# Performance work log

Hardware: AMD Instinct MI355X
Metric: run time of the kernel (lower is better)

The kernel has to match this reference:

```python
import jax, jax.numpy as jnp
import numpy as np
import math

EMBED = 1024
FF = 4096
HEADS = 16
HEAD = EMBED // HEADS
EPS = 1e-5


def new_gelu(x):
    c = math.sqrt(2.0 / math.pi)
    return 0.5 * x * (1.0 + jnp.tanh(c * (x + 0.044715 * x ** 3)))


def layer_norm(x, g, b):
    mu = jnp.mean(x, axis=-1, keepdims=True)
    var = jnp.var(x, axis=-1, keepdims=True)
    return (x - mu) * jax.lax.rsqrt(var + EPS) * g + b


def setup_inputs() -> dict:
    key = jax.random.key(0)
    ks = jax.random.split(key, 16)
    s = 0.02
    d = {
        'x': jax.random.normal(ks[0], (2, 2048, EMBED), jnp.float32),
        'Wq': jax.random.normal(ks[1], (EMBED, EMBED)) * s,
        'bq': jnp.zeros((EMBED,)),
        'Wk': jax.random.normal(ks[2], (EMBED, EMBED)) * s,
        'bk': jnp.zeros((EMBED,)),
        'Wv': jax.random.normal(ks[3], (EMBED, EMBED)) * s,
        'bv': jnp.zeros((EMBED,)),
        'Wp': jax.random.normal(ks[4], (EMBED, EMBED)) * s,
        'bp': jnp.zeros((EMBED,)),
        'W1': jax.random.normal(ks[5], (EMBED, FF)) * s,
        'b1': jnp.zeros((FF,)),
        'W2': jax.random.normal(ks[6], (FF, EMBED)) * s,
        'b2': jnp.zeros((EMBED,)),
        'g1': jnp.ones((EMBED,)), 'be1': jnp.zeros((EMBED,)),
        'g2': jnp.ones((EMBED,)), 'be2': jnp.zeros((EMBED,)),
    }
    return d


def reference(x, Wq, bq, Wk, bk, Wv, bv, Wp, bp, W1, b1, W2, b2, g1, be1, g2, be2):
    B, S, D = x.shape
    h = layer_norm(x, g1, be1)
    # project and split heads: [B,S,D] -> [B,H,S,Hd]
    def heads(y):
        return y.reshape(B, S, HEADS, HEAD).transpose(0, 2, 1, 3)
    Q = heads(h @ Wq + bq)
    K = heads(h @ Wk + bk)
    V = heads(h @ Wv + bv)
    att = jnp.einsum('bhqd,bhkd->bhqk', Q, K) / math.sqrt(HEAD)
    att = jax.nn.softmax(att, axis=-1)
    out = jnp.einsum('bhqk,bhkd->bhqd', att, V)
    out = out.transpose(0, 2, 1, 3).reshape(B, S, D)
    x = x + (out @ Wp + bp)  # dropout p=0 / eval -> identity
    h2 = layer_norm(x, g2, be2)
    x = x + (new_gelu(h2 @ W1 + b1) @ W2 + b2)
    return x
```

## Files before the change

### kernel.cpp

```cpp
#include <hip/hip_runtime.h>
#include <cstdint>


typedef __attribute__((ext_vector_type(8))) short short8;
typedef __attribute__((ext_vector_type(4))) float f32x4;

#define QSCL 0.18033688011112042f

__device__ __forceinline__ float bf2f(unsigned short u) {
    union { unsigned int i; float f; } v; v.i = ((unsigned int)u) << 16; return v.f;
}
__device__ __forceinline__ unsigned short f2bf(float f) {
    union { float f; unsigned int i; } v; v.f = f;
    unsigned int u = v.i;
    u += 0x7fff + ((u >> 16) & 1);
    return (unsigned short)(u >> 16);
}
__device__ __forceinline__ float gelu_f(float x) {
    float u = 0.7978845608028654f * (x + 0.044715f * x * x * x);
    float t = 1.f - 2.f / (__expf(2.f * u) + 1.f);
    return 0.5f * x * (1.f + t);
}
__device__ __forceinline__ void async16(const unsigned short* gp, unsigned short* lp) {
    __builtin_amdgcn_global_load_lds(
        (__attribute__((address_space(1))) void*)(gp),
        (__attribute__((address_space(3))) void*)(lp),
        16, 0, 0);
}

__device__ __forceinline__ void ln_dev(
    const float* __restrict__ x, const float* __restrict__ g,
    const float* __restrict__ b, unsigned short* __restrict__ o,
    int row, float* red)
{
    const int tid = threadIdx.x;
    const float4 v = ((const float4*)(x + (size_t)row * 1024))[tid];
    float f0 = v.x, f1 = v.y, f2 = v.z, f3 = v.w;
    float sum = f0 + f1 + f2 + f3;
    float sq  = f0 * f0 + f1 * f1 + f2 * f2 + f3 * f3;
    for (int off = 1; off < 64; off <<= 1) {
        sum += __shfl_xor(sum, off);
        sq  += __shfl_xor(sq,  off);
    }
    int wv = tid >> 6, ln = tid & 63;
    if (ln == 0) { red[wv] = sum; red[4 + wv] = sq; }
    __syncthreads();
    sum = red[0] + red[1] + red[2] + red[3];
    sq  = red[4] + red[5] + red[6] + red[7];
    float mu  = sum * (1.0f / 1024.0f);
    float var = sq  * (1.0f / 1024.0f) - mu * mu;
    float rsd = rsqrtf(fmaxf(var, 0.f) + 1e-5f);
    const float4 gg = ((const float4*)g)[tid];
    const float4 bb = ((const float4*)b)[tid];
    unsigned short* orow = o + (size_t)row * 1024;
    orow[4 * tid + 0] = f2bf((f0 - mu) * rsd * gg.x + bb.x);
    orow[4 * tid + 1] = f2bf((f1 - mu) * rsd * gg.y + bb.y);
    orow[4 * tid + 2] = f2bf((f2 - mu) * rsd * gg.z + bb.z);
    orow[4 * tid + 3] = f2bf((f3 - mu) * rsd * gg.w + bb.w);
}

__device__ __forceinline__ void transpose_dev(
    const float* __restrict__ in, unsigned short* __restrict__ out,
    int R, int C, int inStride, int bx, int by, unsigned short* tile ,
    float scale)
{
    const int tx = threadIdx.x & 15, ty = threadIdx.x >> 4;
    const int c0 = bx * 64, r0 = by * 64;
#pragma unroll
    for (int i = 0; i < 4; ++i) {
        int r = ty + 16 * i;
        float4 v = *(const float4*)(in + (size_t)(r0 + r) * inStride + c0 + tx * 4);
        tile[r * 70 + tx * 4 + 0] = f2bf(v.x * scale);
        tile[r * 70 + tx * 4 + 1] = f2bf(v.y * scale);
        tile[r * 70 + tx * 4 + 2] = f2bf(v.z * scale);
        tile[r * 70 + tx * 4 + 3] = f2bf(v.w * scale);
    }
    __syncthreads();
#pragma unroll
    for (int i = 0; i < 4; ++i) {
        int c = ty * 4 + i;
        ushort4 o;
        o.x = tile[(tx * 4 + 0) * 70 + c];
        o.y = tile[(tx * 4 + 1) * 70 + c];
        o.z = tile[(tx * 4 + 2) * 70 + c];
        o.w = tile[(tx * 4 + 3) * 70 + c];
        *(ushort4*)(out + (size_t)(c0 + c) * R + r0 + tx * 4) = o;
    }
}

__global__ __launch_bounds__(256) void ln_k(
    const float* __restrict__ x, const float* __restrict__ g,
    const float* __restrict__ b, unsigned short* __restrict__ o)
{
    __shared__ float red[8];
    ln_dev(x, g, b, o, blockIdx.x, red);
}
__global__ __launch_bounds__(256) void transpose_f2b(
    const float* __restrict__ in, unsigned short* __restrict__ out,
    int R, int C, int inStride, float scale)
{
    __shared__ unsigned short tile[64 * 70];
    transpose_dev(in, out, R, C, inStride, blockIdx.x, blockIdx.y, tile, scale);
}

__global__ __launch_bounds__(256) void prep1_k(
    const float* __restrict__ x,
    const float* __restrict__ g1, const float* __restrict__ be1,
    const float* __restrict__ Wq, const float* __restrict__ Wk,
    const float* __restrict__ Wv,
    const float* __restrict__ bq, const float* __restrict__ bk,
    const float* __restrict__ bv,
    unsigned short* __restrict__ hb,
    unsigned short* __restrict__ WTqkv,
    float* __restrict__ bcat)
{
    __shared__ unsigned short smem[64 * 70];
    const int b = blockIdx.x;
    if (b < 4096) {
        ln_dev(x, g1, be1, hb, b, (float*)smem);
    } else if (b < 4096 + 768) {
        int t = b - 4096;
        int w = t >> 8;
        int tt = t & 255;
        const float* W = (w == 0) ? Wq : (w == 1) ? Wk : Wv;
        transpose_dev(W, WTqkv + (size_t)w * 1024 * 1024,
                      1024, 1024, 1024, tt & 15, tt >> 4, smem,
                      (w == 0) ? QSCL : 1.f);
    } else {
        int i = (b - 4096 - 768) * 256 + threadIdx.x;
        float v = (i < 1024) ? bq[i] * QSCL : (i < 2048) ? bk[i - 1024] : bv[i - 2048];
        bcat[i] = v;
    }
}

__global__ __launch_bounds__(256) void prep2_k(
    const float* __restrict__ x1,
    const float* __restrict__ g2, const float* __restrict__ be2,
    const float* __restrict__ W1, const float* __restrict__ W2,
    unsigned short* __restrict__ h2,
    unsigned short* __restrict__ WT1,
    unsigned short* __restrict__ WT2)
{
    __shared__ unsigned short smem[64 * 70];
    const int b = blockIdx.x;
    if (b < 4096) {
        ln_dev(x1, g2, be2, h2, b, (float*)smem);
    } else if (b < 4096 + 1024) {
        int t = b - 4096;
        transpose_dev(W1, WT1, 1024, 4096, 4096, t & 63, t >> 6, smem, 1.f);
    } else {
        int t = b - 4096 - 1024;
        transpose_dev(W2, WT2, 4096, 1024, 1024, t & 15, t >> 4, smem, 1.f);
    }
}

__global__ __launch_bounds__(256) void vt_k(
    const unsigned short* __restrict__ src, int stride,
    unsigned short* __restrict__ Vt)
{
    __shared__ unsigned short tile[64][70];
    const int tx = threadIdx.x & 15, ty = threadIdx.x >> 4;
    const int t0 = blockIdx.x * 64;
    const int bh = blockIdx.y;
    const int bo = (bh >> 4) * 2048;
    const int ho = (bh & 15) * 64;
    const unsigned short* s = src + (size_t)bo * stride + ho;
#pragma unroll
    for (int i = 0; i < 4; ++i) {
        int r = ty + 16 * i;
        ushort4 v = *(const ushort4*)(s + (size_t)(t0 + r) * stride + tx * 4);
        tile[r][tx * 4 + 0] = v.x;
        tile[r][tx * 4 + 1] = v.y;
        tile[r][tx * 4 + 2] = v.z;
        tile[r][tx * 4 + 3] = v.w;
    }
    __syncthreads();
    unsigned short* dst = Vt + (size_t)bh * 64 * 2048;
#pragma unroll
    for (int i = 0; i < 4; ++i) {
        int d = ty * 4 + i;
        int u = tx;
        ushort4 o;
        o.x = tile[u +  0][d];
        o.y = tile[u + 16][d];
        o.z = tile[u + 32][d];
        o.w = tile[u + 48][d];
        *(ushort4*)(dst + (size_t)d * 2048 + t0 + u * 4) = o;
    }
}

__global__ __launch_bounds__(256, 3) void gemm_bt(
    const unsigned short* __restrict__ A,
    const unsigned short* __restrict__ Bt,
    const float* __restrict__ bias,
    const float* __restrict__ res,
    void* __restrict__ C,
    int M, int N, int K, int ldb, int dogelu, int out32, float bscale)
{
    __shared__ unsigned short sA[2 * 128 * 32];
    __shared__ unsigned short sB[2 * 128 * 32];
    const int tid  = threadIdx.x;
    const int wave = tid >> 6;
    const int lane = tid & 63;
    const int quad = lane >> 4;
    const int l15  = lane & 15;
    const int bm = blockIdx.y * 128;
    const int bn = blockIdx.x * 128;
    const int wM = (wave >> 1) * 64;
    const int wN = (wave & 1) * 64;

    f32x4 acc[4][4];
#pragma unroll
    for (int i = 0; i < 4; ++i)
#pragma unroll
        for (int j = 0; j < 4; ++j)
            acc[i][j] = (f32x4){0.f, 0.f, 0.f, 0.f};

    const int rowS = tid >> 2;
    const int kcS  = (tid & 3) * 8;
    const unsigned short* gA  = A  + (size_t)(bm + rowS) * K + kcS;
    const unsigned short* gA2 = gA + (size_t)64 * K;
    const unsigned short* gB  = Bt + (size_t)(bn + rowS) * ldb + kcS;
    const unsigned short* gB2 = gB + (size_t)64 * ldb;
    unsigned short* lA  = sA + tid * 8;
    unsigned short* lA2 = lA + 64 * 32;
    unsigned short* lB  = sB + tid * 8;
    unsigned short* lB2 = lB + 64 * 32;

    for (int k0 = 0; k0 < K; k0 += 64) {
        __syncthreads();
        async16(gA + k0,       lA);
        async16(gA2 + k0,      lA2);
        async16(gA + k0 + 32,  lA + 4096);
        async16(gA2 + k0 + 32, lA2 + 4096);
        async16(gB + k0,       lB);
        async16(gB2 + k0,      lB2);
        async16(gB + k0 + 32,  lB + 4096);
        async16(gB2 + k0 + 32, lB2 + 4096);
        __syncthreads();

#pragma unroll
        for (int p = 0; p < 2; ++p) {
            short8 aF[4], bF[4];
#pragma unroll
            for (int mi = 0; mi < 4; ++mi)
                aF[mi] = *(const short8*)(sA + p * 4096 + (wM + mi * 16 + l15) * 32 + quad * 8);
#pragma unroll
            for (int ni = 0; ni < 4; ++ni)
                bF[ni] = *(const short8*)(sB + p * 4096 + (wN + ni * 16 + l15) * 32 + quad * 8);
#pragma unroll
            for (int mi = 0; mi < 4; ++mi)
#pragma unroll
                for (int ni = 0; ni < 4; ++ni)
                    acc[mi][ni] = __builtin_amdgcn_mfma_f32_16x16x32_bf16(
                        aF[mi], bF[ni], acc[mi][ni], 0, 0, 0);
        }
    }

#pragma unroll
    for (int ni = 0; ni < 4; ++ni) {
        int col = bn + wN + ni * 16 + l15;
        float bv = bias ? bias[col] * bscale : 0.f;
#pragma unroll
        for (int mi = 0; mi < 4; ++mi) {
            int row = bm + wM + mi * 16 + quad * 4;
#pragma unroll
            for (int r = 0; r < 4; ++r) {
                float v = acc[mi][ni][r] + bv;
                if (dogelu) v = gelu_f(v);
                size_t idx = (size_t)(row + r) * N + col;
                if (res) v += res[idx];
                if (out32) ((float*)C)[idx] = v;
                else       ((unsigned short*)C)[idx] = f2bf(v);
            }
        }
    }
}

__global__ __launch_bounds__(256, 2) void gemm_bt64(
    const unsigned short* __restrict__ A,
    const unsigned short* __restrict__ Bt,
    const float* __restrict__ bias,
    const float* __restrict__ res,
    void* __restrict__ C,
    int M, int N, int K, int ldb, int dogelu, int out32)
{
    __shared__ unsigned short sA[2 * 128 * 32];
    __shared__ unsigned short sB[2 * 64 * 32];
    const int tid  = threadIdx.x;
    const int wave = tid >> 6;
    const int lane = tid & 63;
    const int quad = lane >> 4;
    const int l15  = lane & 15;
    const int bm = blockIdx.y * 128;
    const int bn = blockIdx.x * 64;
    const int wM = wave * 32;

    f32x4 acc[2][4];
#pragma unroll
    for (int i = 0; i < 2; ++i)
#pragma unroll
        for (int j = 0; j < 4; ++j)
            acc[i][j] = (f32x4){0.f, 0.f, 0.f, 0.f};

    const int rowS = tid >> 2;
    const int kcS  = (tid & 3) * 8;
    const unsigned short* gA  = A  + (size_t)(bm + rowS) * K + kcS;
    const unsigned short* gA2 = gA + (size_t)64 * K;
    const unsigned short* gB  = Bt + (size_t)(bn + rowS) * ldb + kcS;
    unsigned short* lA  = sA + tid * 8;
    unsigned short* lA2 = lA + 64 * 32;
    unsigned short* lB  = sB + tid * 8;

    for (int k0 = 0; k0 < K; k0 += 64) {
        __syncthreads();
        async16(gA + k0,       lA);
        async16(gA2 + k0,      lA2);
        async16(gA + k0 + 32,  lA + 4096);
        async16(gA2 + k0 + 32, lA2 + 4096);
        async16(gB + k0,       lB);
        async16(gB + k0 + 32,  lB + 2048);
        __syncthreads();

#pragma unroll
        for (int p = 0; p < 2; ++p) {
            short8 aF[2], bF[4];
#pragma unroll
            for (int mi = 0; mi < 2; ++mi)
                aF[mi] = *(const short8*)(sA + p * 4096 + (wM + mi * 16 + l15) * 32 + quad * 8);
#pragma unroll
            for (int ni = 0; ni < 4; ++ni)
                bF[ni] = *(const short8*)(sB + p * 2048 + (ni * 16 + l15) * 32 + quad * 8);
#pragma unroll
            for (int mi = 0; mi < 2; ++mi)
#pragma unroll
                for (int ni = 0; ni < 4; ++ni)
                    acc[mi][ni] = __builtin_amdgcn_mfma_f32_16x16x32_bf16(
                        aF[mi], bF[ni], acc[mi][ni], 0, 0, 0);
        }
    }

#pragma unroll
    for (int ni = 0; ni < 4; ++ni) {
        int col = bn + ni * 16 + l15;
        float bv = bias ? bias[col] : 0.f;
#pragma unroll
        for (int mi = 0; mi < 2; ++mi) {
            int row = bm + wM + mi * 16 + quad * 4;
#pragma unroll
            for (int r = 0; r < 4; ++r) {
                float v = acc[mi][ni][r] + bv;
                if (dogelu) v = gelu_f(v);
                size_t idx = (size_t)(row + r) * N + col;
                if (res) v += res[idx];
                if (out32) ((float*)C)[idx] = v;
                else       ((unsigned short*)C)[idx] = f2bf(v);
            }
        }
    }
}

__global__ __launch_bounds__(512, 2) void attn_k(
    const unsigned short* __restrict__ Q,
    const unsigned short* __restrict__ K,
    const unsigned short* __restrict__ Vt,
    unsigned short* __restrict__ O, int qs)
{
    __shared__ unsigned short smem[45056];
    unsigned short* sK = smem;
    unsigned short* sV = smem + 2 * 5632;
    unsigned short* sP = smem + 4 * 5632;

    const int tid  = threadIdx.x;
    const int wave = tid >> 6;
    const int g    = wave & 3;
    const int h    = wave >> 2;
    const int lane = tid & 63;
    const int quad = lane >> 4;
    const int l15  = lane & 15;
    const int qb = blockIdx.x * 256;
    const int bh = blockIdx.y;
    const int bo = (bh >> 4) * 2048;
    const int ho = (bh & 15) * 64;

    const unsigned short* Qb  = Q  + (size_t)bo * qs + ho;
    const unsigned short* Kb  = K  + (size_t)bo * qs + ho;
    const unsigned short* Vtb = Vt + (size_t)bh * 64 * 2048;
    unsigned short* sPg = sP + g * 5632;
    const int ni0 = 2 * h;

    short8 qF[2][4];
#pragma unroll
    for (int ks = 0; ks < 2; ++ks)
#pragma unroll
        for (int mi = 0; mi < 4; ++mi)
            qF[ks][mi] = *(const short8*)(Qb +
                (size_t)(qb + g * 64 + mi * 16 + l15) * qs + ks * 32 + quad * 8);

    short8 onesF;
#pragma unroll
    for (int j = 0; j < 8; ++j) onesF[j] = (short)0x3F80;

    f32x4 accO[4][4];
    f32x4 accL[4];
#pragma unroll
    for (int mi = 0; mi < 4; ++mi) {
        accL[mi] = (f32x4){0.f, 0.f, 0.f, 0.f};
#pragma unroll
        for (int nd = 0; nd < 4; ++nd) accO[mi][nd] = (f32x4){0.f, 0.f, 0.f, 0.f};
    }

    const int rowS = tid >> 3;
    const int dcS  = (tid & 7) * 8;

    short8 kr, vr;
    kr = *(const short8*)(Kb + (size_t)rowS * qs + dcS);
    vr = *(const short8*)(Vtb + (size_t)rowS * 2048 + dcS);
    *(short8*)(sK + rowS * 88 + dcS) = kr;
    *(short8*)(sV + rowS * 88 + dcS) = vr;
    kr = *(const short8*)(Kb + (size_t)(64 + rowS) * qs + dcS);
    vr = *(const short8*)(Vtb + (size_t)rowS * 2048 + 64 + dcS);

    for (int kt = 0; kt < 2048; kt += 64) {
        const int buf = (kt >> 6) & 1;
        __syncthreads();

        short8 bK[2][2];
#pragma unroll
        for (int ks = 0; ks < 2; ++ks)
#pragma unroll
            for (int nj = 0; nj < 2; ++nj)
                bK[ks][nj] = *(const short8*)(sK + buf * 5632 +
                    ((ni0 + nj) * 16 + l15) * 88 + ks * 32 + quad * 8);

#pragma unroll
        for (int mi = 0; mi < 4; ++mi) {
            f32x4 s0 = (f32x4){0.f, 0.f, 0.f, 0.f};
            f32x4 s1 = s0;
#pragma unroll
            for (int ks = 0; ks < 2; ++ks) {
                s0 = __builtin_amdgcn_mfma_f32_16x16x32_bf16(qF[ks][mi], bK[ks][0], s0, 0, 0, 0);
                s1 = __builtin_amdgcn_mfma_f32_16x16x32_bf16(qF[ks][mi], bK[ks][1], s1, 0, 0, 0);
            }
#pragma unroll
            for (int r = 0; r < 4; ++r) {
                float p0 = __builtin_amdgcn_exp2f(s0[r]);
                float p1 = __builtin_amdgcn_exp2f(s1[r]);
                unsigned int w;
                asm("v_cvt_pk_bf16_f32 %0, %1, %2" : "=v"(w) : "v"(p0), "v"(p1));
                *(unsigned int*)(sPg + (mi * 16 + quad * 4 + r) * 88 + l15 * 4 + ni0) = w;
            }
        }

        __syncthreads();

        short8 aP[4], bV[4];
#pragma unroll
        for (int nd = 0; nd < 4; ++nd)
            bV[nd] = *(const short8*)(sV + buf * 5632 + (nd * 16 + l15) * 88 + h * 32 + quad * 8);
#pragma unroll
        for (int mi = 0; mi < 4; ++mi)
            aP[mi] = *(const short8*)(sPg + (mi * 16 + l15) * 88 + h * 32 + quad * 8);

        if (kt + 64 < 2048) {
            *(short8*)(sK + (buf ^ 1) * 5632 + rowS * 88 + dcS) = kr;
            *(short8*)(sV + (buf ^ 1) * 5632 + rowS * 88 + dcS) = vr;
            if (kt + 128 < 2048) {
                kr = *(const short8*)(Kb + (size_t)(kt + 128 + rowS) * qs + dcS);
                vr = *(const short8*)(Vtb + (size_t)rowS * 2048 + kt + 128 + dcS);
            }
        }

        __builtin_amdgcn_s_setprio(1);
#pragma unroll
        for (int mi = 0; mi < 4; ++mi) {
#pragma unroll
            for (int nd = 0; nd < 4; ++nd)
                accO[mi][nd] = __builtin_amdgcn_mfma_f32_16x16x32_bf16(
                    aP[mi], bV[nd], accO[mi][nd], 0, 0, 0);
            accL[mi] = __builtin_amdgcn_mfma_f32_16x16x32_bf16(
                aP[mi], onesF, accL[mi], 0, 0, 0);
        }
        __builtin_amdgcn_s_setprio(0);
    }

    __syncthreads();
    float* scr = (float*)smem;
    float* po = scr + (size_t)(g * 64 + lane) * 68;
    float* pl = scr + 17408 + (size_t)(g * 64 + lane) * 20;
    if (h == 1) {
#pragma unroll
        for (int mi = 0; mi < 4; ++mi) {
#pragma unroll
            for (int nd = 0; nd < 4; ++nd)
                *(f32x4*)(po + mi * 16 + nd * 4) = accO[mi][nd];
            *(f32x4*)(pl + mi * 4) = accL[mi];
        }
    }
    __syncthreads();
    if (h == 0) {
#pragma unroll
        for (int mi = 0; mi < 4; ++mi) {
            accL[mi] += *(const f32x4*)(pl + mi * 4);
#pragma unroll
            for (int nd = 0; nd < 4; ++nd)
                accO[mi][nd] += *(const f32x4*)(po + mi * 16 + nd * 4);
        }
#pragma unroll
        for (int mi = 0; mi < 4; ++mi)
#pragma unroll
            for (int r = 0; r < 4; ++r) {
                int row = qb + g * 64 + mi * 16 + quad * 4 + r;
                float inv = 1.f / accL[mi][r];
#pragma unroll
                for (int nd = 0; nd < 4; ++nd)
                    O[(size_t)(bo + row) * 1024 + ho + nd * 16 + l15] =
                        f2bf(accO[mi][nd][r] * inv);
            }
    }
}

extern "C" void kernel_launch(void* const* d_in, const int* in_sizes, int n_in,
                              void* d_out, int out_size, void* d_ws, size_t ws_size,
                              hipStream_t stream)
{
    (void)in_sizes; (void)n_in; (void)out_size;
    const float* x   = (const float*)d_in[0];
    const float* Wq  = (const float*)d_in[1];
    const float* bq  = (const float*)d_in[2];
    const float* Wk  = (const float*)d_in[3];
    const float* bk  = (const float*)d_in[4];
    const float* Wv  = (const float*)d_in[5];
    const float* bv  = (const float*)d_in[6];
    const float* Wp  = (const float*)d_in[7];
    const float* bp  = (const float*)d_in[8];
    const float* W1  = (const float*)d_in[9];
    const float* b1  = (const float*)d_in[10];
    const float* W2  = (const float*)d_in[11];
    const float* b2  = (const float*)d_in[12];
    const float* g1  = (const float*)d_in[13];
    const float* be1 = (const float*)d_in[14];
    const float* g2  = (const float*)d_in[15];
    const float* be2 = (const float*)d_in[16];
    float* out = (float*)d_out;

    char* ws = (char*)d_ws;
    char* dob = (char*)d_out;
    const size_t MB = 1024 * 1024;

    if (ws_size >= 40 * MB) {
        unsigned short* hb    = (unsigned short*)dob;
        unsigned short* WTqkv = (unsigned short*)(dob + 8 * MB);
        float*          bcat  = (float*)(dob + 14 * MB);
        unsigned short* QKV   = (unsigned short*)ws;
        unsigned short* att   = (unsigned short*)(ws + 24 * MB);
        unsigned short* Vt    = (unsigned short*)(ws + 32 * MB);
        unsigned short* WTp   = (unsigned short*)(ws + 32 * MB);
        unsigned short* h2    = (unsigned short*)ws;
        unsigned short* WT1   = (unsigned short*)(ws + 8 * MB);
        unsigned short* WT2   = (unsigned short*)(ws + 16 * MB);
        unsigned short* act   = (unsigned short*)(ws + 24 * MB);

        prep1_k<<<4096 + 768 + 12, 256, 0, stream>>>(
            x, g1, be1, Wq, Wk, Wv, bq, bk, bv, hb, WTqkv, bcat);
        gemm_bt<<<dim3(24, 32), 256, 0, stream>>>(hb, WTqkv, bcat, nullptr, QKV,
                                                  4096, 3072, 1024, 1024, 0, 0, 1.f);
        vt_k<<<dim3(32, 32), 256, 0, stream>>>(QKV + 2048, 3072, Vt);
        attn_k<<<dim3(8, 32), 512, 0, stream>>>(QKV, QKV + 1024, Vt, att, 3072);
        transpose_f2b<<<dim3(16, 16), 256, 0, stream>>>(Wp, WTp, 1024, 1024, 1024, 1.f);
        gemm_bt64<<<dim3(16, 32), 256, 0, stream>>>(att, WTp, bp, x, out,
                                                    4096, 1024, 1024, 1024, 0, 1);
        prep2_k<<<4096 + 2048, 256, 0, stream>>>(out, g2, be2, W1, W2, h2, WT1, WT2);
        for (int c = 0; c < 2; ++c) {
            gemm_bt<<<dim3(16, 32), 256, 0, stream>>>(h2, WT1 + (size_t)c * 2048 * 1024,
                                                      b1 + c * 2048, nullptr, act,
                                                      4096, 2048, 1024, 1024, 1, 0, 1.f);
            gemm_bt64<<<dim3(16, 32), 256, 0, stream>>>(act, WT2 + (size_t)c * 2048,
                                                        c == 0 ? b2 : nullptr, out, out,
                                                        4096, 1024, 2048, 4096, 0, 1);
        }
    } else {
        unsigned short* Qw  = (unsigned short*)(ws);
        unsigned short* Kw  = (unsigned short*)(ws + 8 * MB);
        unsigned short* Vw  = (unsigned short*)(ws + 16 * MB);
        unsigned short* hb  = (unsigned short*)dob;
        unsigned short* WTq = (unsigned short*)(dob + 8 * MB);
        unsigned short* VtF = (unsigned short*)(dob + 8 * MB);
        unsigned short* att = Qw;
        unsigned short* WTb = Kw;
        unsigned short* h2  = Vw;
        unsigned short* act = Qw;

        ln_k<<<4096, 256, 0, stream>>>(x, g1, be1, hb);
        transpose_f2b<<<dim3(16, 16), 256, 0, stream>>>(Wq, WTq, 1024, 1024, 1024, QSCL);
        gemm_bt<<<dim3(8, 32), 256, 0, stream>>>(hb, WTq, bq, nullptr, Qw, 4096, 1024, 1024, 1024, 0, 0, QSCL);
        transpose_f2b<<<dim3(16, 16), 256, 0, stream>>>(Wk, WTq, 1024, 1024, 1024, 1.f);
        gemm_bt<<<dim3(8, 32), 256, 0, stream>>>(hb, WTq, bk, nullptr, Kw, 4096, 1024, 1024, 1024, 0, 0, 1.f);
        transpose_f2b<<<dim3(16, 16), 256, 0, stream>>>(Wv, WTq, 1024, 1024, 1024, 1.f);
        gemm_bt<<<dim3(8, 32), 256, 0, stream>>>(hb, WTq, bv, nullptr, Vw, 4096, 1024, 1024, 1024, 0, 0, 1.f);
        vt_k<<<dim3(32, 32), 256, 0, stream>>>(Vw, 1024, VtF);
        attn_k<<<dim3(8, 32), 512, 0, stream>>>(Qw, Kw, VtF, att, 1024);
        transpose_f2b<<<dim3(16, 16), 256, 0, stream>>>(Wp, WTb, 1024, 1024, 1024, 1.f);
        gemm_bt64<<<dim3(16, 32), 256, 0, stream>>>(att, WTb, bp, x, out, 4096, 1024, 1024, 1024, 0, 1);
        ln_k<<<4096, 256, 0, stream>>>(out, g2, be2, h2);
        for (int c = 0; c < 4; ++c) {
            transpose_f2b<<<dim3(16, 16), 256, 0, stream>>>(W1 + c * 1024, WTb, 1024, 1024, 4096, 1.f);
            gemm_bt64<<<dim3(16, 32), 256, 0, stream>>>(h2, WTb, b1 + c * 1024, nullptr, act,
                                                        4096, 1024, 1024, 1024, 1, 0);
            unsigned short* WT2c = WTb + 1024 * 1024;
            transpose_f2b<<<dim3(16, 16), 256, 0, stream>>>(W2 + (size_t)c * 1024 * 1024, WT2c,
                                                            1024, 1024, 1024, 1.f);
            gemm_bt64<<<dim3(16, 32), 256, 0, stream>>>(act, WT2c, c == 0 ? b2 : nullptr,
                                                        out, out, 4096, 1024, 1024, 1024, 0, 1);
        }
    }
}
```

Measured before the change: 378.0 us.

## Drop attention P barrier, deepen gemm_bt64 k-step, reorder V transpose writes

```diff
diff --git a/kernel.cpp b/kernel.cpp
--- a/kernel.cpp
+++ b/kernel.cpp
@@ -176,16 +176,17 @@
     }
     __syncthreads();
     unsigned short* dst = Vt + (size_t)bh * 64 * 2048;
+    const int hh = tx >> 3;
+    const int uu = (tx & 7) * 2;
 #pragma unroll
     for (int i = 0; i < 4; ++i) {
         int d = ty * 4 + i;
-        int u = tx;
         ushort4 o;
-        o.x = tile[u +  0][d];
-        o.y = tile[u + 16][d];
-        o.z = tile[u + 32][d];
-        o.w = tile[u + 48][d];
-        *(ushort4*)(dst + (size_t)d * 2048 + t0 + u * 4) = o;
+        o.x = tile[32 * hh + uu][d];
+        o.y = tile[32 * hh + 16 + uu][d];
+        o.z = tile[32 * hh + uu + 1][d];
+        o.w = tile[32 * hh + 17 + uu][d];
+        *(ushort4*)(dst + (size_t)d * 2048 + t0 + tx * 4) = o;
     }
 }
 
@@ -285,8 +286,8 @@
     void* __restrict__ C,
     int M, int N, int K, int ldb, int dogelu, int out32)
 {
-    __shared__ unsigned short sA[2 * 128 * 32];
-    __shared__ unsigned short sB[2 * 64 * 32];
+    __shared__ unsigned short sA[4 * 128 * 32];
+    __shared__ unsigned short sB[4 * 64 * 32];
     const int tid  = threadIdx.x;
     const int wave = tid >> 6;
     const int lane = tid & 63;
@@ -312,18 +313,18 @@
     unsigned short* lA2 = lA + 64 * 32;
     unsigned short* lB  = sB + tid * 8;
 
-    for (int k0 = 0; k0 < K; k0 += 64) {
+    for (int k0 = 0; k0 < K; k0 += 128) {
         __syncthreads();
-        async16(gA + k0,       lA);
-        async16(gA2 + k0,      lA2);
-        async16(gA + k0 + 32,  lA + 4096);
-        async16(gA2 + k0 + 32, lA2 + 4096);
-        async16(gB + k0,       lB);
-        async16(gB + k0 + 32,  lB + 2048);
+#pragma unroll
+        for (int p = 0; p < 4; ++p) {
+            async16(gA  + k0 + p * 32, lA  + p * 4096);
+            async16(gA2 + k0 + p * 32, lA2 + p * 4096);
+            async16(gB  + k0 + p * 32, lB  + p * 2048);
+        }
         __syncthreads();
 
 #pragma unroll
-        for (int p = 0; p < 2; ++p) {
+        for (int p = 0; p < 4; ++p) {
             short8 aF[2], bF[4];
 #pragma unroll
             for (int mi = 0; mi < 2; ++mi)
@@ -433,34 +434,17 @@
                 bK[ks][nj] = *(const short8*)(sK + buf * 5632 +
                     ((ni0 + nj) * 16 + l15) * 88 + ks * 32 + quad * 8);
 
+        f32x4 s0[4], s1[4];
 #pragma unroll
         for (int mi = 0; mi < 4; ++mi) {
-            f32x4 s0 = (f32x4){0.f, 0.f, 0.f, 0.f};
-            f32x4 s1 = s0;
+            s0[mi] = (f32x4){0.f, 0.f, 0.f, 0.f};
+            s1[mi] = s0[mi];
 #pragma unroll
             for (int ks = 0; ks < 2; ++ks) {
-                s0 = __builtin_amdgcn_mfma_f32_16x16x32_bf16(qF[ks][mi], bK[ks][0], s0, 0, 0, 0);
-                s1 = __builtin_amdgcn_mfma_f32_16x16x32_bf16(qF[ks][mi], bK[ks][1], s1, 0, 0, 0);
+                s0[mi] = __builtin_amdgcn_mfma_f32_16x16x32_bf16(qF[ks][mi], bK[ks][0], s0[mi], 0, 0, 0);
+                s1[mi] = __builtin_amdgcn_mfma_f32_16x16x32_bf16(qF[ks][mi], bK[ks][1], s1[mi], 0, 0, 0);
             }
-#pragma unroll
-            for (int r = 0; r < 4; ++r) {
-                float p0 = __builtin_amdgcn_exp2f(s0[r]);
-                float p1 = __builtin_amdgcn_exp2f(s1[r]);
-                unsigned int w;
-                asm("v_cvt_pk_bf16_f32 %0, %1, %2" : "=v"(w) : "v"(p0), "v"(p1));
-                *(unsigned int*)(sPg + (mi * 16 + quad * 4 + r) * 88 + l15 * 4 + ni0) = w;
-            }
-        }
-
-        __syncthreads();
-
-        short8 aP[4], bV[4];
-#pragma unroll
-        for (int nd = 0; nd < 4; ++nd)
-            bV[nd] = *(const short8*)(sV + buf * 5632 + (nd * 16 + l15) * 88 + h * 32 + quad * 8);
-#pragma unroll
-        for (int mi = 0; mi < 4; ++mi)
-            aP[mi] = *(const short8*)(sPg + (mi * 16 + l15) * 88 + h * 32 + quad * 8);
+        }
 
         if (kt + 64 < 2048) {
             *(short8*)(sK + (buf ^ 1) * 5632 + rowS * 88 + dcS) = kr;
@@ -470,6 +454,25 @@
                 vr = *(const short8*)(Vtb + (size_t)rowS * 2048 + kt + 128 + dcS);
             }
         }
+
+#pragma unroll
+        for (int mi = 0; mi < 4; ++mi)
+#pragma unroll
+            for (int r = 0; r < 4; ++r) {
+                float p0 = __builtin_amdgcn_exp2f(s0[mi][r]);
+                float p1 = __builtin_amdgcn_exp2f(s1[mi][r]);
+                unsigned int w;
+                asm("v_cvt_pk_bf16_f32 %0, %1, %2" : "=v"(w) : "v"(p0), "v"(p1));
+                *(unsigned int*)(sPg + (mi * 16 + quad * 4 + r) * 88 + h * 32 + l15 * 2) = w;
+            }
+
+        short8 aP[4], bV[4];
+#pragma unroll
+        for (int nd = 0; nd < 4; ++nd)
+            bV[nd] = *(const short8*)(sV + buf * 5632 + (nd * 16 + l15) * 88 + h * 32 + quad * 8);
+#pragma unroll
+        for (int mi = 0; mi < 4; ++mi)
+            aP[mi] = *(const short8*)(sPg + (mi * 16 + l15) * 88 + h * 32 + quad * 8);
 
         __builtin_amdgcn_s_setprio(1);
 #pragma unroll
```

Result: no change. 379.6 us (+0.4%).
